# Kernel optimization log

Hardware: AMD Instinct MI355X
Metric: run time of the kernel (lower is better)

Reference implementation:

```python
import jax, jax.numpy as jnp
import numpy as np

EPS = 1e-12  # F.normalize eps
WIN_SIZE = 200
WIN_STEP = 30  # eval mode (training uses 10)
N_WIN = 30     # 31 windows from length-1100 axis, last one dropped


def setup_inputs() -> dict:
    key = jax.random.key(0)
    ks = jax.random.split(key, 6)
    dim, K, out_dim = 128, 64, 256
    N, H, W = 8, 16, 900
    s = 1.0 / np.sqrt(dim)
    return {
        "x": jax.random.normal(ks[0], (N, dim, H, W), dtype=jnp.float32),
        "cluster_centers": jax.random.uniform(ks[1], (K, dim), dtype=jnp.float32),
        "conv_w": jax.random.normal(ks[2], (K, dim), dtype=jnp.float32) * s,
        "conv_b": jax.random.normal(ks[3], (K,), dtype=jnp.float32) * s,
        "mlp_w": jax.random.normal(ks[4], (out_dim, K * dim), dtype=jnp.float32) * s,
        "mlp_b": jax.random.normal(ks[5], (out_dim,), dtype=jnp.float32) * s,
    }


def _l2norm(v, axis):
    return v / jnp.clip(jnp.linalg.norm(v, axis=axis, keepdims=True), EPS)


def reference(x, cluster_centers, conv_w, conv_b, mlp_w, mlp_b):
    N, C, H, W = x.shape
    K = conv_w.shape[0]
    # 1x1 conv -> soft assignment, softmax over clusters (dim=1 after view(N,K,HW))
    logits = jnp.einsum('nchw,kc->nkhw', x, conv_w) + conv_b[None, :, None, None]
    a = jax.nn.softmax(logits, axis=1)  # (N,K,H,W)
    # Fused weighted residual sum over H (torch sums dim=-2 of (N,K,C,H,W)):
    # vlad_pre[n,k,c,w] = sum_h a[n,k,h,w]*x[n,c,h,w] - centers[k,c]*sum_h a[n,k,h,w]
    wx = jnp.einsum('nkhw,nchw->nkcw', a, x)               # (N,K,C,W)
    asum = a.sum(axis=2)                                    # (N,K,W)
    res = wx - cluster_centers[None, :, :, None] * asum[:, :, None, :]
    # circular pad along yaw: [800:] ++ all ++ [:100] -> length 1100
    res = jnp.concatenate([res[..., 800:], res, res[..., :100]], axis=-1)
    # sliding-window sum, size 200 step 30, drop last window -> 30 windows
    cs = jnp.cumsum(res, axis=-1)
    cs = jnp.concatenate([jnp.zeros(res.shape[:-1] + (1,), res.dtype), cs], axis=-1)
    starts = jnp.arange(N_WIN) * WIN_STEP
    win = cs[..., starts + WIN_SIZE] - cs[..., starts]      # (N,K,C,30)
    vlad = jnp.transpose(win, (0, 3, 1, 2)).reshape(N * N_WIN, K, C)
    vlad = _l2norm(vlad, axis=2)                            # intra-norm per cluster
    vlad = _l2norm(vlad.reshape(N * N_WIN, K * C), axis=1)  # global norm
    out = vlad @ mlp_w.T + mlp_b
    out = _l2norm(out, axis=1)
    return out.reshape(N, N_WIN, -1)
```

## Files before the change

### kernel.cpp

```cpp
#include <hip/hip_runtime.h>
#include <cstddef>

#define EPSF 1e-12f
#define NCB 90
#define NT 30
#define ODIM 256
#define DDIM 8192

typedef unsigned short u16;
typedef __attribute__((ext_vector_type(8))) short short8;
typedef __attribute__((ext_vector_type(4))) float float4v;

__device__ inline u16 f2bf(float f) {
  union { float f; unsigned u; } v; v.f = f;
  unsigned r = v.u + 0x7FFFu + ((v.u >> 16) & 1u);
  return (u16)(r >> 16);
}
__device__ inline float bf2f(u16 h) {
  union { unsigned u; float f; } v; v.u = ((unsigned)h) << 16;
  return v.f;
}

__global__ __launch_bounds__(512, 2) void k1_assign(
    const float* __restrict__ x,
    const float* __restrict__ conv_w,
    const float* __restrict__ conv_b,
    float* __restrict__ P,
    float* __restrict__ PA)
{
  __shared__ u16 xtf[4160];
  __shared__ u16 xf[5120];
  __shared__ float As[64 * 33];
  __shared__ u16 afr[2048];
  __shared__ float invs[32];
  __shared__ float pasum[512];

  const int bx0 = blockIdx.x;
  const int n = bx0 & 7;
  const int cb = bx0 >> 3;
  const int t = threadIdx.x;
  const int lane = t & 63;
  const int w8 = t >> 6;

  const float* xn = x + (size_t)n * 1843200 + cb * 10;

  const int colt = w8 & 1;
  const int kt = w8 >> 1;
  const int kr = kt * 16 + (lane & 15);
  const float bk = conv_b[kr];

  short8 wh[4], wl[4];
  {
    const int cbase = (lane >> 4) << 3;
#pragma unroll
    for (int cb32 = 0; cb32 < 4; ++cb32) {
      const float* wp = conv_w + (size_t)kr * 128 + cb32 * 32 + cbase;
      float4 u0 = *(const float4*)wp;
      float4 u1 = *(const float4*)(wp + 4);
      float fv[8] = {u0.x, u0.y, u0.z, u0.w, u1.x, u1.y, u1.z, u1.w};
      union { u16 u[8]; short8 v; } hh, ll;
#pragma unroll
      for (int j = 0; j < 8; ++j) {
        u16 h = f2bf(fv[j]);
        hh.u[j] = h;
        ll.u[j] = f2bf(fv[j] - bf2f(h));
      }
      wh[cb32] = hh.v; wl[cb32] = ll.v;
    }
  }

  float4v pacc[4];
#pragma unroll
  for (int i = 0; i < 4; ++i) pacc[i] = (float4v){0.f, 0.f, 0.f, 0.f};
  float pak = 0.f;

  float2 xr[4];
#pragma unroll
  for (int s = 0; s < 4; ++s) {
    int e2 = t + 512 * s;
    int c = e2 >> 4, p = e2 & 15;
    int cl = 2 * p;
    int h = cl / 10, wi = cl - 10 * h;
    xr[s] = *(const float2*)(xn + (size_t)c * 14400 + h * 900 + wi);
  }

  for (int cc = 0; cc < 5; ++cc) {
    __syncthreads();
#pragma unroll
    for (int s = 0; s < 4; ++s) {
      int e2 = t + 512 * s;
      int c = e2 >> 4, p = e2 & 15;
      int cl = 2 * p;
      u16 h0 = f2bf(xr[s].x), h1 = f2bf(xr[s].y);
      int ip = (c >> 4) * 640 + (p >> 2) * 160 + (c & 15) * 8 + (cl & 7);
      ushort2 pr; pr.x = h0; pr.y = h1;
      *(ushort2*)&xf[ip] = pr;
      int F = (p >> 3) * 4 + (c >> 5);
      int L = (((c >> 3) & 3) << 4) + (cl & 15);
      int i0 = F * 520 + L * 8 + (c & 7);
      xtf[i0] = h0;
      xtf[i0 + 8] = h1;
    }
    if (cc < 4) {
#pragma unroll
      for (int s = 0; s < 4; ++s) {
        int e2 = t + 512 * s;
        int c = e2 >> 4, p = e2 & 15;
        int g = (cc + 1) * 32 + 2 * p;
        int h = g / 10, wi = g - 10 * h;
        xr[s] = *(const float2*)(xn + (size_t)c * 14400 + h * 900 + wi);
      }
    }
    __syncthreads();

    {
      float4v d0 = (float4v){0.f, 0.f, 0.f, 0.f};
#pragma unroll
      for (int cb32 = 0; cb32 < 4; ++cb32) {
        short8 xa = *(short8*)&xtf[(colt * 4 + cb32) * 520 + lane * 8];
        d0 = __builtin_amdgcn_mfma_f32_16x16x32_bf16(xa, wh[cb32], d0, 0, 0, 0);
        d0 = __builtin_amdgcn_mfma_f32_16x16x32_bf16(xa, wl[cb32], d0, 0, 0, 0);
      }
      int colb = colt * 16 + ((lane >> 4) << 2);
#pragma unroll
      for (int r = 0; r < 4; ++r)
        As[kr * 33 + colb + r] = d0[r] + bk;
    }
    __syncthreads();

    {
      const int col4 = lane & 3;
      const int kq = lane >> 2;
      const int colg = w8 * 4 + col4;
      float m = -3.4e38f;
#pragma unroll
      for (int i = 0; i < 4; ++i) m = fmaxf(m, As[(kq * 4 + i) * 33 + colg]);
      m = fmaxf(m, __shfl_xor(m, 4));
      m = fmaxf(m, __shfl_xor(m, 8));
      m = fmaxf(m, __shfl_xor(m, 16));
      m = fmaxf(m, __shfl_xor(m, 32));
      float s = 0.f;
#pragma unroll
      for (int i = 0; i < 4; ++i) {
        int a = (kq * 4 + i) * 33 + colg;
        float e = __expf(As[a] - m);
        As[a] = e;
        s += e;
      }
      s += __shfl_xor(s, 4);
      s += __shfl_xor(s, 8);
      s += __shfl_xor(s, 16);
      s += __shfl_xor(s, 32);
      if (kq == 0) invs[colg] = 1.f / s;
    }
    {
      union { u16 u[4]; ushort4 v; } cvt;
      float paks = 0.f;
#pragma unroll
      for (int j = 0; j < 4; ++j) {
        float a = As[lane * 33 + w8 * 4 + j] * invs[w8 * 4 + j];
        paks += a;
        cvt.u[j] = f2bf(a);
      }
      pak += paks;
      int dst = ((lane >> 4) * 64 + ((w8 >> 1) << 4) + (lane & 15)) * 8 + (w8 & 1) * 4;
      *(ushort4*)&afr[dst] = cvt.v;
    }
    __syncthreads();

    {
      short8 aa = *(short8*)&afr[((w8 >> 1) * 64 + lane) * 8];
#pragma unroll
      for (int c4 = 0; c4 < 4; ++c4) {
        int ct = (w8 & 1) * 4 + c4;
        short8 xb = *(short8*)&xf[ct * 640 + (lane >> 4) * 160 + (lane & 15) * 8];
        pacc[c4] = __builtin_amdgcn_mfma_f32_16x16x32_bf16(aa, xb, pacc[c4], 0, 0, 0);
      }
    }
  }

  float* Pp = P + (size_t)(n * NCB + cb) * DDIM;
  {
    int krow = (w8 >> 1) * 16 + ((lane >> 4) << 2);
    int c0 = (w8 & 1) * 64 + (lane & 15);
#pragma unroll
    for (int c4 = 0; c4 < 4; ++c4)
#pragma unroll
      for (int r = 0; r < 4; ++r)
        Pp[(krow + r) * 128 + c0 + c4 * 16] = pacc[c4][r];
  }
  pasum[t] = pak;
  __syncthreads();
  if (t < 64) {
    float s = 0.f;
#pragma unroll
    for (int i = 0; i < 8; ++i) s += pasum[t + 64 * i];
    PA[(size_t)(n * NCB + cb) * 64 + t] = s;
  }
}

__global__ __launch_bounds__(256) void k2_vlad(
    const float* __restrict__ P, const float* __restrict__ PA,
    const float* __restrict__ centers, u16* __restrict__ vlad16,
    float* __restrict__ gss)
{
  __shared__ float Ak[8];
  __shared__ float red[4];
  const int bx0 = blockIdx.x;
  const int id = (bx0 & 7) * 240 + (bx0 >> 3);
  const int n = id / 240;
  const int rem = id - n * 240;
  const int wt = rem >> 3, eb = rem & 7;
  const int win = n * NT + wt;
  const int t = threadIdx.x;

  if (t < 32) {
    int kk = t >> 2, ii = t & 3;
    float s = 0.f;
#pragma unroll
    for (int ss = 0; ss < 5; ++ss) {
      int i = ii + 4 * ss;
      int cb = (3 * wt + 80 + i) % 90;
      s += PA[((size_t)n * NCB + cb) * 64 + eb * 8 + kk];
    }
    s += __shfl_xor(s, 1);
    s += __shfl_xor(s, 2);
    if (ii == 0) Ak[kk] = s;
  }
  __syncthreads();

  const int e0 = eb * 1024 + t * 4;
  const float* base = P + (size_t)n * NCB * DDIM + e0;
  float v[4];
#pragma unroll
  for (int j = 0; j < 4; ++j) v[j] = 0.f;
#pragma unroll 5
  for (int i = 0; i < 20; ++i) {
    int cb = (3 * wt + 80 + i) % 90;
    float4 u0 = *(const float4*)(base + (size_t)cb * DDIM);
    v[0] += u0.x; v[1] += u0.y; v[2] += u0.z; v[3] += u0.w;
  }

  const float A = Ak[t >> 5];
  const float* ce = centers + e0;
  float ss8 = 0.f;
#pragma unroll
  for (int j = 0; j < 4; ++j) {
    float val = v[j] - ce[j] * A;
    v[j] = val;
    ss8 += val * val;
  }
  float ssg = ss8;
  ssg += __shfl_xor(ssg, 1);
  ssg += __shfl_xor(ssg, 2);
  ssg += __shfl_xor(ssg, 4);
  ssg += __shfl_xor(ssg, 8);
  ssg += __shfl_xor(ssg, 16);
  float rn = 1.f / fmaxf(sqrtf(ssg), EPSF);
  float ts = ss8 * rn * rn;
  ts += __shfl_xor(ts, 1);
  ts += __shfl_xor(ts, 2);
  ts += __shfl_xor(ts, 4);
  ts += __shfl_xor(ts, 8);
  ts += __shfl_xor(ts, 16);
  ts += __shfl_xor(ts, 32);
  if ((t & 63) == 0) red[t >> 6] = ts;
  __syncthreads();
  if (t == 0) gss[(size_t)win * 8 + eb] = red[0] + red[1] + red[2] + red[3];

  union { u16 u[4]; ushort4 v4; } o;
#pragma unroll
  for (int j = 0; j < 4; ++j) o.u[j] = f2bf(v[j] * rn);
  *(ushort4*)(vlad16 + (size_t)win * DDIM + e0) = o.v4;
}

__global__ __launch_bounds__(256) void k3_gemm(
    const u16* __restrict__ vlad16, const float* __restrict__ gss,
    const float* __restrict__ mlp_w, float* __restrict__ part)
{
  __shared__ float ga[48];
  const int bx = blockIdx.x;
  const int xcd = bx & 7;
  const int q = bx >> 3;
  const int rtg = q % 5;
  const int h = (q / 5) * 8 + xcd;
  const int ot = h & 1;
  const int ks = h >> 1;
  const int t = threadIdx.x;
  const int lane = t & 63;
  const int w = t >> 6;

  if (t < 48) {
    int r = rtg * 48 + t;
    float s = 0.f;
#pragma unroll
    for (int j = 0; j < 8; ++j) s += gss[(size_t)r * 8 + j];
    ga[t] = 1.f / fmaxf(sqrtf(s), EPSF);
  }
  __syncthreads();

  const int m = lane & 15;
  const int kg = lane >> 4;
  const int d0 = ks * 256 + kg * 8;
  const u16* a0 = vlad16 + (size_t)(rtg * 48 + m) * DDIM + d0;

  float4v acc[3][2];
#pragma unroll
  for (int mi = 0; mi < 3; ++mi)
#pragma unroll
    for (int i = 0; i < 2; ++i) acc[mi][i] = (float4v){0.f, 0.f, 0.f, 0.f};

#pragma unroll
  for (int ko = 0; ko < 8; ++ko) {
    short8 a[3];
#pragma unroll
    for (int mi = 0; mi < 3; ++mi)
      a[mi] = *(const short8*)(a0 + (size_t)(mi * 16) * DDIM + ko * 32);
#pragma unroll
    for (int nt = 0; nt < 2; ++nt) {
      int o = ot * 128 + w * 32 + nt * 16 + m;
      const float* wrow = mlp_w + (size_t)o * DDIM + d0 + ko * 32;
      float4 u0 = *(const float4*)wrow;
      float4 u1 = *(const float4*)(wrow + 4);
      union { u16 u[8]; short8 v; } bb;
      bb.u[0] = f2bf(u0.x); bb.u[1] = f2bf(u0.y); bb.u[2] = f2bf(u0.z); bb.u[3] = f2bf(u0.w);
      bb.u[4] = f2bf(u1.x); bb.u[5] = f2bf(u1.y); bb.u[6] = f2bf(u1.z); bb.u[7] = f2bf(u1.w);
#pragma unroll
      for (int mi = 0; mi < 3; ++mi)
        acc[mi][nt] = __builtin_amdgcn_mfma_f32_16x16x32_bf16(a[mi], bb.v, acc[mi][nt], 0, 0, 0);
    }
  }

  float* pp = part + ((size_t)ks * 240 + rtg * 48) * ODIM;
#pragma unroll
  for (int mi = 0; mi < 3; ++mi)
#pragma unroll
    for (int nt = 0; nt < 2; ++nt) {
      int o = ot * 128 + w * 32 + nt * 16 + m;
#pragma unroll
      for (int r = 0; r < 4; ++r) {
        int rl = mi * 16 + kg * 4 + r;
        pp[rl * ODIM + o] = acc[mi][nt][r] * ga[rl];
      }
    }
}

__global__ __launch_bounds__(1024) void k4_out(
    const float* __restrict__ part, const float* __restrict__ bias,
    float* __restrict__ out)
{
  __shared__ float acc[4][256];
  __shared__ float red[4];
  const int r = blockIdx.x;
  const int t = threadIdx.x;
  const int o = t & 255, sq = t >> 8;

  float v = 0.f;
#pragma unroll
  for (int s = 0; s < 8; ++s)
    v += part[((size_t)(sq * 8 + s) * 240 + r) * ODIM + o];
  acc[sq][o] = v;
  __syncthreads();

  float ss = 0.f;
  if (t < 256) {
    v = acc[0][o] + acc[1][o] + acc[2][o] + acc[3][o] + bias[o];
    ss = v * v;
    ss += __shfl_xor(ss, 32);
    ss += __shfl_xor(ss, 16);
    ss += __shfl_xor(ss, 8);
    ss += __shfl_xor(ss, 4);
    ss += __shfl_xor(ss, 2);
    ss += __shfl_xor(ss, 1);
    if ((t & 63) == 0) red[t >> 6] = ss;
  }
  __syncthreads();
  if (t < 256) {
    float total = red[0] + red[1] + red[2] + red[3];
    out[(size_t)r * ODIM + o] = v / fmaxf(sqrtf(total), EPSF);
  }
}

extern "C" void kernel_launch(void* const* d_in, const int* in_sizes, int n_in,
                              void* d_out, int out_size, void* d_ws, size_t ws_size,
                              hipStream_t stream) {
  const float* x       = (const float*)d_in[0];
  const float* centers = (const float*)d_in[1];
  const float* conv_w  = (const float*)d_in[2];
  const float* conv_b  = (const float*)d_in[3];
  const float* mlp_w   = (const float*)d_in[4];
  const float* mlp_b   = (const float*)d_in[5];
  float* out = (float*)d_out;

  float* ws     = (float*)d_ws;
  float* P      = ws;
  float* PA     = ws + 5898240;
  u16*   vlad16 = (u16*)(ws + 5944320);
  float* gss    = (float*)(ws + 6927360);
  float* part   = ws;

  k1_assign<<<dim3(8 * NCB),    dim3(512),  0, stream>>>(x, conv_w, conv_b, P, PA);
  k2_vlad  <<<dim3(8 * NT * 8), dim3(256),  0, stream>>>(P, PA, centers, vlad16, gss);
  k3_gemm  <<<dim3(320),        dim3(256),  0, stream>>>(vlad16, gss, mlp_w, part);
  k4_out   <<<dim3(240),        dim3(1024), 0, stream>>>(part, mlp_b, out);
}
```

Measured before the change: 161.7 us.

## Process three column blocks per k1 block to amortize weight setup and syncs

k1_assign now handles three adjacent 10-column slabs per workgroup, with 240 blocks instead of 720. Each slab gets its own region of one large shared buffer and its own accumulators. The conv-weight bf16 split and the barriers are shared across the three slabs, and more loads are in flight per thread. In exchange, register pressure and shared memory (about 81KB) grow, which likely lowers occupancy, and there are fewer blocks to spread across CUs. A small change in k4 swaps the reduction-lane test from t to o.

```diff
diff --git a/kernel.cpp b/kernel.cpp
--- a/kernel.cpp
+++ b/kernel.cpp
@@ -28,21 +28,16 @@
     float* __restrict__ P,
     float* __restrict__ PA)
 {
-  __shared__ u16 xtf[4160];
-  __shared__ u16 xf[5120];
-  __shared__ float As[64 * 33];
-  __shared__ u16 afr[2048];
-  __shared__ float invs[32];
-  __shared__ float pasum[512];
+  __shared__ __align__(16) char smem[81408];
 
   const int bx0 = blockIdx.x;
   const int n = bx0 & 7;
-  const int cb = bx0 >> 3;
+  const int q = bx0 >> 3;
   const int t = threadIdx.x;
   const int lane = t & 63;
   const int w8 = t >> 6;
 
-  const float* xn = x + (size_t)n * 1843200 + cb * 10;
+  const float* xn0 = x + (size_t)n * 1843200 + (size_t)(3 * q) * 10;
 
   const int colt = w8 & 1;
   const int kt = w8 >> 1;
@@ -69,19 +64,24 @@
     }
   }
 
-  float4v pacc[4];
-#pragma unroll
-  for (int i = 0; i < 4; ++i) pacc[i] = (float4v){0.f, 0.f, 0.f, 0.f};
-  float pak = 0.f;
-
-  float2 xr[4];
+  float4v pacc[3][4];
+#pragma unroll
+  for (int si = 0; si < 3; ++si)
+#pragma unroll
+    for (int i = 0; i < 4; ++i) pacc[si][i] = (float4v){0.f, 0.f, 0.f, 0.f};
+  float pak[3] = {0.f, 0.f, 0.f};
+
+  float2 xr[3][4];
 #pragma unroll
   for (int s = 0; s < 4; ++s) {
     int e2 = t + 512 * s;
     int c = e2 >> 4, p = e2 & 15;
     int cl = 2 * p;
     int h = cl / 10, wi = cl - 10 * h;
-    xr[s] = *(const float2*)(xn + (size_t)c * 14400 + h * 900 + wi);
+    const float* ap = xn0 + (size_t)c * 14400 + h * 900 + wi;
+#pragma unroll
+    for (int si = 0; si < 3; ++si)
+      xr[si][s] = *(const float2*)(ap + si * 10);
   }
 
   for (int cc = 0; cc < 5; ++cc) {
@@ -91,15 +91,20 @@
       int e2 = t + 512 * s;
       int c = e2 >> 4, p = e2 & 15;
       int cl = 2 * p;
-      u16 h0 = f2bf(xr[s].x), h1 = f2bf(xr[s].y);
       int ip = (c >> 4) * 640 + (p >> 2) * 160 + (c & 15) * 8 + (cl & 7);
-      ushort2 pr; pr.x = h0; pr.y = h1;
-      *(ushort2*)&xf[ip] = pr;
       int F = (p >> 3) * 4 + (c >> 5);
       int L = (((c >> 3) & 3) << 4) + (cl & 15);
       int i0 = F * 520 + L * 8 + (c & 7);
-      xtf[i0] = h0;
-      xtf[i0 + 8] = h1;
+#pragma unroll
+      for (int si = 0; si < 3; ++si) {
+        u16 h0 = f2bf(xr[si][s].x), h1 = f2bf(xr[si][s].y);
+        u16* xf = (u16*)(smem + si * 27136 + 8320);
+        u16* xtf = (u16*)(smem + si * 27136);
+        ushort2 pr; pr.x = h0; pr.y = h1;
+        *(ushort2*)&xf[ip] = pr;
+        xtf[i0] = h0;
+        xtf[i0 + 8] = h1;
+      }
     }
     if (cc < 4) {
 #pragma unroll
@@ -108,94 +113,126 @@
         int c = e2 >> 4, p = e2 & 15;
         int g = (cc + 1) * 32 + 2 * p;
         int h = g / 10, wi = g - 10 * h;
-        xr[s] = *(const float2*)(xn + (size_t)c * 14400 + h * 900 + wi);
+        const float* ap = xn0 + (size_t)c * 14400 + h * 900 + wi;
+#pragma unroll
+        for (int si = 0; si < 3; ++si)
+          xr[si][s] = *(const float2*)(ap + si * 10);
       }
     }
     __syncthreads();
 
     {
-      float4v d0 = (float4v){0.f, 0.f, 0.f, 0.f};
+      float4v d0[3];
+#pragma unroll
+      for (int si = 0; si < 3; ++si) d0[si] = (float4v){0.f, 0.f, 0.f, 0.f};
 #pragma unroll
       for (int cb32 = 0; cb32 < 4; ++cb32) {
-        short8 xa = *(short8*)&xtf[(colt * 4 + cb32) * 520 + lane * 8];
-        d0 = __builtin_amdgcn_mfma_f32_16x16x32_bf16(xa, wh[cb32], d0, 0, 0, 0);
-        d0 = __builtin_amdgcn_mfma_f32_16x16x32_bf16(xa, wl[cb32], d0, 0, 0, 0);
+#pragma unroll
+        for (int si = 0; si < 3; ++si) {
+          const u16* xtf = (const u16*)(smem + si * 27136);
+          short8 xa = *(short8*)&xtf[(colt * 4 + cb32) * 520 + lane * 8];
+          d0[si] = __builtin_amdgcn_mfma_f32_16x16x32_bf16(xa, wh[cb32], d0[si], 0, 0, 0);
+          d0[si] = __builtin_amdgcn_mfma_f32_16x16x32_bf16(xa, wl[cb32], d0[si], 0, 0, 0);
+        }
       }
       int colb = colt * 16 + ((lane >> 4) << 2);
 #pragma unroll
-      for (int r = 0; r < 4; ++r)
-        As[kr * 33 + colb + r] = d0[r] + bk;
+      for (int si = 0; si < 3; ++si) {
+        float* As = (float*)(smem + si * 27136 + 18560);
+#pragma unroll
+        for (int r = 0; r < 4; ++r)
+          As[kr * 33 + colb + r] = d0[si][r] + bk;
+      }
     }
     __syncthreads();
 
-    {
-      const int col4 = lane & 3;
-      const int kq = lane >> 2;
-      const int colg = w8 * 4 + col4;
-      float m = -3.4e38f;
-#pragma unroll
-      for (int i = 0; i < 4; ++i) m = fmaxf(m, As[(kq * 4 + i) * 33 + colg]);
-      m = fmaxf(m, __shfl_xor(m, 4));
-      m = fmaxf(m, __shfl_xor(m, 8));
-      m = fmaxf(m, __shfl_xor(m, 16));
-      m = fmaxf(m, __shfl_xor(m, 32));
-      float s = 0.f;
-#pragma unroll
-      for (int i = 0; i < 4; ++i) {
-        int a = (kq * 4 + i) * 33 + colg;
-        float e = __expf(As[a] - m);
-        As[a] = e;
-        s += e;
-      }
-      s += __shfl_xor(s, 4);
-      s += __shfl_xor(s, 8);
-      s += __shfl_xor(s, 16);
-      s += __shfl_xor(s, 32);
-      if (kq == 0) invs[colg] = 1.f / s;
-    }
-    {
-      union { u16 u[4]; ushort4 v; } cvt;
-      float paks = 0.f;
-#pragma unroll
-      for (int j = 0; j < 4; ++j) {
-        float a = As[lane * 33 + w8 * 4 + j] * invs[w8 * 4 + j];
-        paks += a;
-        cvt.u[j] = f2bf(a);
-      }
-      pak += paks;
-      int dst = ((lane >> 4) * 64 + ((w8 >> 1) << 4) + (lane & 15)) * 8 + (w8 & 1) * 4;
-      *(ushort4*)&afr[dst] = cvt.v;
+#pragma unroll
+    for (int si = 0; si < 3; ++si) {
+      float* As = (float*)(smem + si * 27136 + 18560);
+      float* invs = (float*)(smem + si * 27136 + 27008);
+      u16* afr = (u16*)(smem + si * 27136);
+      {
+        const int col4 = lane & 3;
+        const int kq = lane >> 2;
+        const int colg = w8 * 4 + col4;
+        float m = -3.4e38f;
+#pragma unroll
+        for (int i = 0; i < 4; ++i) m = fmaxf(m, As[(kq * 4 + i) * 33 + colg]);
+        m = fmaxf(m, __shfl_xor(m, 4));
+        m = fmaxf(m, __shfl_xor(m, 8));
+        m = fmaxf(m, __shfl_xor(m, 16));
+        m = fmaxf(m, __shfl_xor(m, 32));
+        float s = 0.f;
+#pragma unroll
+        for (int i = 0; i < 4; ++i) {
+          int a = (kq * 4 + i) * 33 + colg;
+          float e = __expf(As[a] - m);
+          As[a] = e;
+          s += e;
+        }
+        s += __shfl_xor(s, 4);
+        s += __shfl_xor(s, 8);
+        s += __shfl_xor(s, 16);
+        s += __shfl_xor(s, 32);
+        if (kq == 0) invs[colg] = 1.f / s;
+      }
+      {
+        union { u16 u[4]; ushort4 v; } cvt;
+        float paks = 0.f;
+#pragma unroll
+        for (int j = 0; j < 4; ++j) {
+          float a = As[lane * 33 + w8 * 4 + j] * invs[w8 * 4 + j];
+          paks += a;
+          cvt.u[j] = f2bf(a);
+        }
+        pak[si] += paks;
+        int dst = ((lane >> 4) * 64 + ((w8 >> 1) << 4) + (lane & 15)) * 8 + (w8 & 1) * 4;
+        *(ushort4*)&afr[dst] = cvt.v;
+      }
     }
     __syncthreads();
 
-    {
+#pragma unroll
+    for (int si = 0; si < 3; ++si) {
+      const u16* afr = (const u16*)(smem + si * 27136);
+      const u16* xf = (const u16*)(smem + si * 27136 + 8320);
       short8 aa = *(short8*)&afr[((w8 >> 1) * 64 + lane) * 8];
 #pragma unroll
       for (int c4 = 0; c4 < 4; ++c4) {
         int ct = (w8 & 1) * 4 + c4;
         short8 xb = *(short8*)&xf[ct * 640 + (lane >> 4) * 160 + (lane & 15) * 8];
-        pacc[c4] = __builtin_amdgcn_mfma_f32_16x16x32_bf16(aa, xb, pacc[c4], 0, 0, 0);
-      }
-    }
-  }
-
-  float* Pp = P + (size_t)(n * NCB + cb) * DDIM;
+        pacc[si][c4] = __builtin_amdgcn_mfma_f32_16x16x32_bf16(aa, xb, pacc[si][c4], 0, 0, 0);
+      }
+    }
+  }
+
   {
     int krow = (w8 >> 1) * 16 + ((lane >> 4) << 2);
     int c0 = (w8 & 1) * 64 + (lane & 15);
 #pragma unroll
-    for (int c4 = 0; c4 < 4; ++c4)
-#pragma unroll
-      for (int r = 0; r < 4; ++r)
-        Pp[(krow + r) * 128 + c0 + c4 * 16] = pacc[c4][r];
-  }
-  pasum[t] = pak;
+    for (int si = 0; si < 3; ++si) {
+      float* Pp = P + (size_t)(n * NCB + 3 * q + si) * DDIM;
+#pragma unroll
+      for (int c4 = 0; c4 < 4; ++c4)
+#pragma unroll
+        for (int r = 0; r < 4; ++r)
+          Pp[(krow + r) * 128 + c0 + c4 * 16] = pacc[si][c4][r];
+    }
+  }
+  __syncthreads();
+#pragma unroll
+  for (int si = 0; si < 3; ++si)
+    ((float*)(smem + si * 27136 + 18560))[t] = pak[si];
   __syncthreads();
   if (t < 64) {
-    float s = 0.f;
-#pragma unroll
-    for (int i = 0; i < 8; ++i) s += pasum[t + 64 * i];
-    PA[(size_t)(n * NCB + cb) * 64 + t] = s;
+#pragma unroll
+    for (int si = 0; si < 3; ++si) {
+      const float* pasum = (const float*)(smem + si * 27136 + 18560);
+      float s = 0.f;
+#pragma unroll
+      for (int i = 0; i < 8; ++i) s += pasum[t + 64 * i];
+      PA[(size_t)(n * NCB + 3 * q + si) * 64 + t] = s;
+    }
   }
 }
 
@@ -372,7 +409,7 @@
     ss += __shfl_xor(ss, 4);
     ss += __shfl_xor(ss, 2);
     ss += __shfl_xor(ss, 1);
-    if ((t & 63) == 0) red[t >> 6] = ss;
+    if ((o & 63) == 0) red[t >> 6] = ss;
   }
   __syncthreads();
   if (t < 256) {
@@ -399,7 +436,7 @@
   float* gss    = (float*)(ws + 6927360);
   float* part   = ws;
 
-  k1_assign<<<dim3(8 * NCB),    dim3(512),  0, stream>>>(x, conv_w, conv_b, P, PA);
+  k1_assign<<<dim3(240),        dim3(512),  0, stream>>>(x, conv_w, conv_b, P, PA);
   k2_vlad  <<<dim3(8 * NT * 8), dim3(256),  0, stream>>>(P, PA, centers, vlad16, gss);
   k3_gemm  <<<dim3(320),        dim3(256),  0, stream>>>(vlad16, gss, mlp_w, part);
   k4_out   <<<dim3(240),        dim3(1024), 0, stream>>>(part, mlp_b, out);
```

New measurement: 154.7 us. 4.3% less time.
